# Kernel optimization log

Measured on AMD Instinct MI355X. Metric: run time of the kernel, lower is better.

Reference implementation:

```python
import jax, jax.numpy as jnp
import numpy as np

B, T, C = 2, 2048, 1024
NH = 16
HD = C // NH

def setup_inputs() -> dict:
    key = jax.random.key(0)
    ks = jax.random.split(key, 4)
    x = jax.random.normal(ks[0], (B, T, C), dtype=jnp.float32)
    w_attn = jax.random.normal(ks[1], (C, 3 * C), dtype=jnp.float32) * (1.0 / np.sqrt(C))
    b_attn = jnp.zeros((3 * C,), dtype=jnp.float32)
    w_proj = jax.random.normal(ks[2], (C, C), dtype=jnp.float32) * (1.0 / np.sqrt(C))
    b_proj = jnp.zeros((C,), dtype=jnp.float32)
    return {"x": x, "w_attn": w_attn, "b_attn": b_attn, "w_proj": w_proj, "b_proj": b_proj}

def reference(x, w_attn, b_attn, w_proj, b_proj):
    Bq, Tq, Cq = x.shape
    qkv = x @ w_attn + b_attn                      # [B,T,3C]
    q, k, v = jnp.split(qkv, 3, axis=2)
    # [B,T,C] -> [B,NH,T,HD]
    def heads(t):
        return t.reshape(Bq, Tq, NH, HD).transpose(0, 2, 1, 3)
    q, k, v = heads(q), heads(k), heads(v)
    att = jnp.einsum('bhqd,bhkd->bhqk', q, k) * (1.0 / np.sqrt(HD))
    causal = jnp.tril(jnp.ones((Tq, Tq), dtype=bool))
    att = jnp.where(causal[None, None], att, -jnp.inf)
    att = jax.nn.softmax(att, axis=-1)
    y = jnp.einsum('bhqk,bhkd->bhqd', att, v)      # [B,NH,T,HD]
    y = y.transpose(0, 2, 1, 3).reshape(Bq, Tq, Cq)
    return y @ w_proj + b_proj
```

## Files before the change

### kernel.cpp

```cpp
#include <hip/hip_runtime.h>

typedef unsigned short u16;
typedef short bf16x8 __attribute__((ext_vector_type(8)));
typedef float f32x4 __attribute__((ext_vector_type(4)));

#define BATCH 2
#define SEQ   2048
#define CH    1024
#define NHEAD 16
#define HDIM  64
#define ROWS  (BATCH*SEQ)

#define SWZ(r_, c_) (((r_)*64) + ((c_) ^ (((r_)&7)*8)))

__device__ __forceinline__ u16 f2b(float f) {
  unsigned u = __builtin_bit_cast(unsigned, f);
  u += 0x7FFFu + ((u >> 16) & 1u);
  return (u16)(u >> 16);
}
__device__ __forceinline__ float b2f(u16 h) {
  unsigned u = ((unsigned)h) << 16;
  return __builtin_bit_cast(float, u);
}
__device__ __forceinline__ float exp2_fast(float x) {
  float r; asm("v_exp_f32 %0, %1" : "=v"(r) : "v"(x)); return r;
}
__device__ __forceinline__ unsigned cvt_pk_bf16(float a, float b) {
  unsigned r; asm("v_cvt_pk_bf16_f32 %0, %1, %2" : "=v"(r) : "v"(a), "v"(b)); return r;
}

__device__ __forceinline__ void gload_lds16(const void* g, void* l) {
  __builtin_amdgcn_global_load_lds(
      (const __attribute__((address_space(1))) unsigned int*)g,
      (__attribute__((address_space(3))) unsigned int*)l, 16, 0, 0);
}

__global__ void csa_convert_x(const float* __restrict__ in, u16* __restrict__ out,
                              int n8) {
  int i = blockIdx.x * 256 + threadIdx.x;
  if (i >= n8) return;
  const float4* f4 = (const float4*)in;
  float4 v0 = f4[2*i], v1 = f4[2*i+1];
  ushort4 o0, o1;
  o0.x = f2b(v0.x); o0.y = f2b(v0.y); o0.z = f2b(v0.z); o0.w = f2b(v0.w);
  o1.x = f2b(v1.x); o1.y = f2b(v1.y); o1.z = f2b(v1.z); o1.w = f2b(v1.w);
  ((ushort4*)out)[2*i]   = o0;
  ((ushort4*)out)[2*i+1] = o1;
}

__global__ void csa_transpose2(const float* __restrict__ wa, const float* __restrict__ wp,
                               u16* __restrict__ wat, u16* __restrict__ wpt) {
  __shared__ float tile[32][33];
  int bx = blockIdx.x;
  const float* in; u16* out; int C;
  if (bx < 96) { in = wa; out = wat; C = 3*CH; }
  else         { in = wp; out = wpt; C = CH; bx -= 96; }
  const int R = CH;
  const int bxc = bx * 32, by = blockIdx.y * 32;
  const int tx = threadIdx.x, ty = threadIdx.y;
  #pragma unroll
  for (int j = 0; j < 4; ++j) {
    int r = by + ty + j*8, c = bxc + tx;
    tile[ty + j*8][tx] = in[(size_t)r*C + c];
  }
  __syncthreads();
  #pragma unroll
  for (int j = 0; j < 4; ++j) {
    int oc = bxc + ty + j*8;
    int orr = by + tx;
    out[(size_t)oc*R + orr] = f2b(tile[tx][ty + j*8]);
  }
}

__global__ __launch_bounds__(512) void csa_gemm_qkv(
    const u16* __restrict__ A, const u16* __restrict__ Bt,
    const float* __restrict__ bias,
    u16* __restrict__ qbo, u16* __restrict__ kb, u16* __restrict__ vtb)
{
  __shared__ __align__(16) u16 As[2][256*64];
  __shared__ __align__(16) u16 Bs[2][192*64];
  const int t = threadIdx.x, lane = t & 63, w = t >> 6;
  const int wm = w >> 2, wn = w & 3, g = lane >> 4, qi = lane & 15;

  const int wgid = blockIdx.y * 16 + blockIdx.x;
  const int c8 = wgid & 7, inner = wgid >> 3;
  const int bm = (c8 >> 1) * 4 + (inner >> 3);
  const int bn = (c8 & 1) * 8 + (inner & 7);

  f32x4 acc[8][3] = {};

  const u16* Ab = A  + (size_t)(bm*256)*CH;
  const u16* Bb = Bt + (size_t)(bn*192)*CH;
  const int srow = t >> 3;
  const int scol = (t & 7) * 8;

  #pragma unroll
  for (int p = 0; p < 4; ++p)
    gload_lds16(Ab + (size_t)(p*64 + srow)*CH + scol, &As[0][p*4096 + w*512]);
  #pragma unroll
  for (int p = 0; p < 3; ++p)
    gload_lds16(Bb + (size_t)(p*64 + srow)*CH + scol, &Bs[0][p*4096 + w*512]);
  __syncthreads();

  int cur = 0;
  for (int k0 = 0; k0 < CH; k0 += 64) {
    if (k0 + 64 < CH) {
      #pragma unroll
      for (int p = 0; p < 4; ++p)
        gload_lds16(Ab + (size_t)(p*64 + srow)*CH + (k0+64) + scol, &As[cur^1][p*4096 + w*512]);
      #pragma unroll
      for (int p = 0; p < 3; ++p)
        gload_lds16(Bb + (size_t)(p*64 + srow)*CH + (k0+64) + scol, &Bs[cur^1][p*4096 + w*512]);
    }
    #pragma unroll
    for (int kk = 0; kk < 2; ++kk) {
      bf16x8 af[8], bfr[3];
      #pragma unroll
      for (int m = 0; m < 8; ++m)
        af[m] = *(const bf16x8*)&As[cur][(wm*128 + m*16 + qi)*64 + kk*32 + g*8];
      #pragma unroll
      for (int n = 0; n < 3; ++n)
        bfr[n] = *(const bf16x8*)&Bs[cur][(wn*48 + n*16 + qi)*64 + kk*32 + g*8];
      #pragma unroll
      for (int m = 0; m < 8; ++m)
        #pragma unroll
        for (int n = 0; n < 3; ++n)
          acc[m][n] = __builtin_amdgcn_mfma_f32_16x16x32_bf16(af[m], bfr[n], acc[m][n], 0, 0, 0);
    }
    __syncthreads();
    cur ^= 1;
  }

  #pragma unroll
  for (int m = 0; m < 8; ++m) {
    const int row0 = bm*256 + wm*128 + m*16 + g*4;
    const int bb = row0 >> 11;
    const int t0 = row0 & 2047;
    #pragma unroll
    for (int n = 0; n < 3; ++n) {
      const int col = bn*192 + wn*48 + n*16 + qi;
      const float bv = bias[col];
      const int which = col >> 10;
      const int cc = col & 1023;
      const int h = cc >> 6, d = cc & 63;
      const int bh = bb*16 + h;
      if (which == 2) {
        ushort4 pw;
        pw.x = f2b(acc[m][n][0] + bv);
        pw.y = f2b(acc[m][n][1] + bv);
        pw.z = f2b(acc[m][n][2] + bv);
        pw.w = f2b(acc[m][n][3] + bv);
        *(ushort4*)&vtb[((size_t)bh*HDIM + d)*SEQ + t0] = pw;
      } else {
        u16* dst = (which == 0) ? qbo : kb;
        #pragma unroll
        for (int r = 0; r < 4; ++r)
          dst[((size_t)bh*SEQ + t0 + r)*HDIM + d] = f2b(acc[m][n][r] + bv);
      }
    }
  }
}

__global__ __launch_bounds__(256) void csa_gemm_proj(
    const u16* __restrict__ A, const u16* __restrict__ Bt,
    const float* __restrict__ bias, float* __restrict__ out)
{
  __shared__ __align__(16) u16 As[2][128*64];
  __shared__ __align__(16) u16 Bs[2][128*64];
  const int t = threadIdx.x, lane = t & 63, w = t >> 6;
  const int wm = w >> 1, wn = w & 1, g = lane >> 4, qi = lane & 15;
  const int bm = blockIdx.y, bn = blockIdx.x;

  f32x4 acc[4][4] = {};

  const u16* Ab = A  + (size_t)(bm*128)*CH;
  const u16* Bb = Bt + (size_t)(bn*128)*CH;
  const int srow = t >> 3;
  const int scol = (t & 7) * 8;

  #pragma unroll
  for (int p = 0; p < 4; ++p) {
    gload_lds16(Ab + (size_t)(p*32 + srow)*CH + scol, &As[0][p*2048 + w*512]);
    gload_lds16(Bb + (size_t)(p*32 + srow)*CH + scol, &Bs[0][p*2048 + w*512]);
  }
  __syncthreads();

  int cur = 0;
  for (int k0 = 0; k0 < CH; k0 += 64) {
    if (k0 + 64 < CH) {
      #pragma unroll
      for (int p = 0; p < 4; ++p) {
        gload_lds16(Ab + (size_t)(p*32 + srow)*CH + (k0+64) + scol, &As[cur^1][p*2048 + w*512]);
        gload_lds16(Bb + (size_t)(p*32 + srow)*CH + (k0+64) + scol, &Bs[cur^1][p*2048 + w*512]);
      }
    }
    #pragma unroll
    for (int kk = 0; kk < 2; ++kk) {
      bf16x8 af[4], bfr[4];
      #pragma unroll
      for (int m = 0; m < 4; ++m)
        af[m] = *(const bf16x8*)&As[cur][(wm*64 + m*16 + qi)*64 + kk*32 + g*8];
      #pragma unroll
      for (int n = 0; n < 4; ++n)
        bfr[n] = *(const bf16x8*)&Bs[cur][(wn*64 + n*16 + qi)*64 + kk*32 + g*8];
      #pragma unroll
      for (int m = 0; m < 4; ++m)
        #pragma unroll
        for (int n = 0; n < 4; ++n)
          acc[m][n] = __builtin_amdgcn_mfma_f32_16x16x32_bf16(af[m], bfr[n], acc[m][n], 0, 0, 0);
    }
    __syncthreads();
    cur ^= 1;
  }

  #pragma unroll
  for (int m = 0; m < 4; ++m) {
    const int row0 = bm*128 + wm*64 + m*16 + g*4;
    #pragma unroll
    for (int n = 0; n < 4; ++n) {
      const int col = bn*128 + wn*64 + n*16 + qi;
      const float bv = bias[col];
      #pragma unroll
      for (int r = 0; r < 4; ++r)
        out[(size_t)(row0 + r)*CH + col] = acc[m][n][r] + bv;
    }
  }
}

__global__ __launch_bounds__(512) void csa_attn(
    const u16* __restrict__ qb, const u16* __restrict__ kb,
    const u16* __restrict__ vtb, u16* __restrict__ yout)
{
  const int bh = blockIdx.x, pair = blockIdx.y;
  const int bidx = bh >> 4, h = bh & 15;
  const int t = threadIdx.x, lane = t & 63, w = t >> 6;
  const int g = lane >> 4, qi = lane & 15;
  __shared__ __align__(16) u16 Ks[2][64*64];
  __shared__ __align__(16) u16 Vs[3][64*64];
  __shared__ __align__(16) u16 Ps[8][16*64];

  const size_t kvbase = (size_t)bh * SEQ * HDIM;
  const int srow = t >> 3;
  const int ssw  = (srow & 7) * 8;
  const int scol = ((t & 7) * 8) ^ ssw;

  int offK[2][4], offPw[4], offPr[2];
  #pragma unroll
  for (int c = 0; c < 2; ++c) {
    offPr[c] = SWZ(qi, c*32 + g*8);
    #pragma unroll
    for (int s4 = 0; s4 < 4; ++s4) offK[c][s4] = SWZ(s4*16 + qi, c*32 + g*8);
  }
  #pragma unroll
  for (int s4 = 0; s4 < 4; ++s4) offPw[s4] = SWZ(qi, s4*16 + g*4);

  const float QSCALE = 0.18033688011112042f;

  for (int half = 0; half < 2; ++half) {
    const int qt = half ? (15 - pair) : pair;
    const int qrow = qt*128 + w*16;
    const int nkt = 2*qt + 2;
    const int kend = qrow >> 6;

    bf16x8 qf[2];
    #pragma unroll
    for (int c = 0; c < 2; ++c) {
      qf[c] = *(const bf16x8*)&qb[(kvbase + (size_t)(qrow + qi)*HDIM) + c*32 + g*8];
      #pragma unroll
      for (int e = 0; e < 8; ++e)
        qf[c][e] = (short)f2b(b2f((u16)qf[c][e]) * QSCALE);
    }

    f32x4 yacc[4] = {};
    float mrun = -1e30f, srun = 0.f;

    gload_lds16(kb  + kvbase + (size_t)srow*HDIM + scol, &Ks[0][w*512]);
    gload_lds16(vtb + kvbase + (size_t)srow*SEQ  + scol, &Vs[0][w*512]);
    __syncthreads();
    if (nkt > 1) {
      gload_lds16(kb  + kvbase + (size_t)(64 + srow)*HDIM + scol, &Ks[1][w*512]);
      gload_lds16(vtb + kvbase + (size_t)srow*SEQ + 64 + scol,    &Vs[1][w*512]);
    }
    f32x4 st[4] = {};
    #pragma unroll
    for (int c = 0; c < 2; ++c)
      #pragma unroll
      for (int s4 = 0; s4 < 4; ++s4) {
        bf16x8 kf = *(const bf16x8*)&Ks[0][offK[c][s4]];
        st[s4] = __builtin_amdgcn_mfma_f32_16x16x32_bf16(kf, qf[c], st[s4], 0, 0, 0);
      }

    int v0i = 0, v2i = 2;
    for (int kt = 0; kt < nkt; ++kt) {
      __syncthreads();

      if (kt + 2 < nkt) {
        const int k2 = (kt + 2) * 64;
        gload_lds16(kb  + kvbase + (size_t)(k2 + srow)*HDIM + scol, &Ks[kt & 1][w*512]);
        gload_lds16(vtb + kvbase + (size_t)srow*SEQ + k2 + scol,    &Vs[v2i][w*512]);
      }

      f32x4 st2[4] = {};
      const bool doqk = (kt + 1 <= kend);
      if (doqk) {
        #pragma unroll
        for (int c = 0; c < 2; ++c)
          #pragma unroll
          for (int s4 = 0; s4 < 4; ++s4) {
            bf16x8 kf = *(const bf16x8*)&Ks[(kt + 1) & 1][offK[c][s4]];
            st2[s4] = __builtin_amdgcn_mfma_f32_16x16x32_bf16(kf, qf[c], st2[s4], 0, 0, 0);
          }
      }

      if (kt <= kend) {
        if (kt == kend) {
          const int lq = (qrow & 63) + qi;
          #pragma unroll
          for (int s4 = 0; s4 < 4; ++s4)
            #pragma unroll
            for (int r = 0; r < 4; ++r)
              if (s4*16 + g*4 + r > lq) st[s4][r] = -3.0e38f;
        }

        float m0 = fmaxf(fmaxf(fmaxf(st[0][0], st[0][1]), st[0][2]), st[0][3]);
        float m1 = fmaxf(fmaxf(fmaxf(st[1][0], st[1][1]), st[1][2]), st[1][3]);
        float m2 = fmaxf(fmaxf(fmaxf(st[2][0], st[2][1]), st[2][2]), st[2][3]);
        float m3 = fmaxf(fmaxf(fmaxf(st[3][0], st[3][1]), st[3][2]), st[3][3]);
        float tmax = fmaxf(fmaxf(fmaxf(m0, m1), m2), m3);

        if (!__all(tmax - mrun <= 11.5f)) {
          float tmf = fmaxf(tmax, __shfl_xor(tmax, 16));
          tmf = fmaxf(tmf, __shfl_xor(tmf, 32));
          float mnew = fmaxf(mrun, tmf);
          float fac = exp2_fast(mrun - mnew);
          #pragma unroll
          for (int r = 0; r < 4; ++r) {
            float fr = __shfl(fac, g*4 + r);
            #pragma unroll
            for (int nf = 0; nf < 4; ++nf) yacc[nf][r] *= fr;
          }
          srun *= fac;
          mrun = mnew;
        }
        float tsum = 0.f;
        #pragma unroll
        for (int s4 = 0; s4 < 4; ++s4)
          #pragma unroll
          for (int r = 0; r < 4; ++r) {
            float pv = exp2_fast(st[s4][r] - mrun);
            st[s4][r] = pv;
            tsum += pv;
          }
        srun += tsum;

        #pragma unroll
        for (int s4 = 0; s4 < 4; ++s4) {
          uint2 pw;
          pw.x = cvt_pk_bf16(st[s4][0], st[s4][1]);
          pw.y = cvt_pk_bf16(st[s4][2], st[s4][3]);
          *(uint2*)&Ps[w][offPw[s4]] = pw;
        }

        __builtin_amdgcn_s_setprio(1);
        #pragma unroll
        for (int c = 0; c < 2; ++c) {
          bf16x8 pa = *(const bf16x8*)&Ps[w][offPr[c]];
          #pragma unroll
          for (int nf = 0; nf < 4; ++nf) {
            bf16x8 vf = *(const bf16x8*)&Vs[v0i][offK[c][nf]];
            yacc[nf] = __builtin_amdgcn_mfma_f32_16x16x32_bf16(pa, vf, yacc[nf], 0, 0, 0);
          }
        }
        __builtin_amdgcn_s_setprio(0);
      }

      if (doqk) {
        #pragma unroll
        for (int s4 = 0; s4 < 4; ++s4) st[s4] = st2[s4];
      }
      v0i = (v0i == 2) ? 0 : v0i + 1;
      v2i = (v2i == 2) ? 0 : v2i + 1;
    }

    float srf = srun + __shfl_xor(srun, 16);
    srf += __shfl_xor(srf, 32);
    #pragma unroll
    for (int r = 0; r < 4; ++r) {
      float sv = __shfl(srf, g*4 + r);
      float inv = 1.f / sv;
      int qg = qrow + g*4 + r;
      #pragma unroll
      for (int nf = 0; nf < 4; ++nf) {
        int d = nf*16 + qi;
        yout[((size_t)bidx*SEQ + qg)*CH + h*HDIM + d] = f2b(yacc[nf][r] * inv);
      }
    }
  }
}

extern "C" void kernel_launch(void* const* d_in, const int* in_sizes, int n_in,
                              void* d_out, int out_size, void* d_ws, size_t ws_size,
                              hipStream_t stream) {
  (void)in_sizes; (void)n_in; (void)out_size; (void)ws_size;
  const float* x      = (const float*)d_in[0];
  const float* w_attn = (const float*)d_in[1];
  const float* b_attn = (const float*)d_in[2];
  const float* w_proj = (const float*)d_in[3];
  const float* b_proj = (const float*)d_in[4];

  char* ws = (char*)d_ws;
  const size_t MB = 1024*1024;
  u16* xb  = (u16*)(ws);
  u16* wat = (u16*)(ws +  8*MB);
  u16* wpt = (u16*)(ws + 14*MB);
  u16* qb  = (u16*)(ws + 16*MB);
  u16* kb  = (u16*)(ws + 24*MB);
  u16* vtb = (u16*)(ws + 32*MB);

  csa_convert_x<<<2048, 256, 0, stream>>>(x, xb, ROWS*CH/8);
  csa_transpose2<<<dim3(128, 32), dim3(32, 8), 0, stream>>>(w_attn, w_proj, wat, wpt);
  csa_gemm_qkv<<<dim3(16, 16), 512, 0, stream>>>(xb, wat, b_attn, qb, kb, vtb);
  csa_attn<<<dim3(32, 8), 512, 0, stream>>>(qb, kb, vtb, xb);
  csa_gemm_proj<<<dim3(8, 32), 256, 0, stream>>>(xb, wpt, b_proj, (float*)d_out);
}
```

Measured before the change: 119.4 us.

## Process 128-key tiles per iteration with double-buffered K/V in attention

Restructures the causal attention loop to process 128 keys per iteration as two 64-key halves, with a simple double buffer for K and V instead of the previous 64-key tile loop with a triple-buffered V and software-pipelined QK. This halves the number of iterations and barriers, and turns the per-tile softmax max and rescale into one pass over 128 keys. In exchange it drops the QK-ahead pipelining and the early skip of fully masked 64-key tiles, so the diagonal tile may do wasted work. It also uses more LDS, which may reduce occupancy.

After: 110.9 us. -7.1%, faster.

```diff
diff --git a/kernel.cpp b/kernel.cpp
--- a/kernel.cpp
+++ b/kernel.cpp
@@ -235,32 +235,41 @@
   const int bidx = bh >> 4, h = bh & 15;
   const int t = threadIdx.x, lane = t & 63, w = t >> 6;
   const int g = lane >> 4, qi = lane & 15;
-  __shared__ __align__(16) u16 Ks[2][64*64];
-  __shared__ __align__(16) u16 Vs[3][64*64];
-  __shared__ __align__(16) u16 Ps[8][16*64];
+  __shared__ __align__(16) u16 Ks[2][128*64];
+  __shared__ __align__(16) u16 Vs[2][64*128];
+  __shared__ __align__(16) u16 Ps[8][2][16*64];
 
   const size_t kvbase = (size_t)bh * SEQ * HDIM;
-  const int srow = t >> 3;
-  const int ssw  = (srow & 7) * 8;
-  const int scol = ((t & 7) * 8) ^ ssw;
-
-  int offK[2][4], offPw[4], offPr[2];
+  const u16* kb_bh  = kb  + kvbase;
+  const u16* vtb_bh = vtb + kvbase;
+
+  const int krow_  = t >> 3;
+  const int kcolsw = ((t & 7) * 8) ^ ((krow_ & 7) * 8);
+  const int vd_    = t >> 4;
+  const int vcolsw = ((t & 15) * 8) ^ ((vd_ & 15) * 8);
+
+  int offKb[2][4], offVb[2][4], offPw[4], offPr[2];
   #pragma unroll
   for (int c = 0; c < 2; ++c) {
-    offPr[c] = SWZ(qi, c*32 + g*8);
-    #pragma unroll
-    for (int s4 = 0; s4 < 4; ++s4) offK[c][s4] = SWZ(s4*16 + qi, c*32 + g*8);
-  }
-  #pragma unroll
-  for (int s4 = 0; s4 < 4; ++s4) offPw[s4] = SWZ(qi, s4*16 + g*4);
+    offPr[c] = qi*64 + ((c*32 + g*8) ^ ((qi & 7) * 8));
+    #pragma unroll
+    for (int s4 = 0; s4 < 4; ++s4)
+      offKb[c][s4] = (s4*16 + qi)*64 + ((c*32 + g*8) ^ ((qi & 7) * 8));
+    #pragma unroll
+    for (int nf = 0; nf < 4; ++nf)
+      offVb[c][nf] = (nf*16 + qi)*128 + ((c*32 + g*8) ^ (qi * 8));
+  }
+  #pragma unroll
+  for (int s4 = 0; s4 < 4; ++s4)
+    offPw[s4] = qi*64 + ((s4*16 + g*4) ^ ((qi & 7) * 8));
 
   const float QSCALE = 0.18033688011112042f;
+  const int lqa = w*16 + qi;
 
   for (int half = 0; half < 2; ++half) {
     const int qt = half ? (15 - pair) : pair;
     const int qrow = qt*128 + w*16;
-    const int nkt = 2*qt + 2;
-    const int kend = qrow >> 6;
+    const int ntile = qt + 1;
 
     bf16x8 qf[2];
     #pragma unroll
@@ -274,112 +283,115 @@
     f32x4 yacc[4] = {};
     float mrun = -1e30f, srun = 0.f;
 
-    gload_lds16(kb  + kvbase + (size_t)srow*HDIM + scol, &Ks[0][w*512]);
-    gload_lds16(vtb + kvbase + (size_t)srow*SEQ  + scol, &Vs[0][w*512]);
     __syncthreads();
-    if (nkt > 1) {
-      gload_lds16(kb  + kvbase + (size_t)(64 + srow)*HDIM + scol, &Ks[1][w*512]);
-      gload_lds16(vtb + kvbase + (size_t)srow*SEQ + 64 + scol,    &Vs[1][w*512]);
-    }
-    f32x4 st[4] = {};
-    #pragma unroll
-    for (int c = 0; c < 2; ++c)
-      #pragma unroll
-      for (int s4 = 0; s4 < 4; ++s4) {
-        bf16x8 kf = *(const bf16x8*)&Ks[0][offK[c][s4]];
-        st[s4] = __builtin_amdgcn_mfma_f32_16x16x32_bf16(kf, qf[c], st[s4], 0, 0, 0);
-      }
-
-    int v0i = 0, v2i = 2;
-    for (int kt = 0; kt < nkt; ++kt) {
-      __syncthreads();
-
-      if (kt + 2 < nkt) {
-        const int k2 = (kt + 2) * 64;
-        gload_lds16(kb  + kvbase + (size_t)(k2 + srow)*HDIM + scol, &Ks[kt & 1][w*512]);
-        gload_lds16(vtb + kvbase + (size_t)srow*SEQ + k2 + scol,    &Vs[v2i][w*512]);
-      }
-
-      f32x4 st2[4] = {};
-      const bool doqk = (kt + 1 <= kend);
-      if (doqk) {
-        #pragma unroll
-        for (int c = 0; c < 2; ++c)
-          #pragma unroll
-          for (int s4 = 0; s4 < 4; ++s4) {
-            bf16x8 kf = *(const bf16x8*)&Ks[(kt + 1) & 1][offK[c][s4]];
-            st2[s4] = __builtin_amdgcn_mfma_f32_16x16x32_bf16(kf, qf[c], st2[s4], 0, 0, 0);
-          }
-      }
-
-      if (kt <= kend) {
-        if (kt == kend) {
-          const int lq = (qrow & 63) + qi;
-          #pragma unroll
-          for (int s4 = 0; s4 < 4; ++s4)
-            #pragma unroll
-            for (int r = 0; r < 4; ++r)
-              if (s4*16 + g*4 + r > lq) st[s4][r] = -3.0e38f;
-        }
-
-        float m0 = fmaxf(fmaxf(fmaxf(st[0][0], st[0][1]), st[0][2]), st[0][3]);
-        float m1 = fmaxf(fmaxf(fmaxf(st[1][0], st[1][1]), st[1][2]), st[1][3]);
-        float m2 = fmaxf(fmaxf(fmaxf(st[2][0], st[2][1]), st[2][2]), st[2][3]);
-        float m3 = fmaxf(fmaxf(fmaxf(st[3][0], st[3][1]), st[3][2]), st[3][3]);
-        float tmax = fmaxf(fmaxf(fmaxf(m0, m1), m2), m3);
-
-        if (!__all(tmax - mrun <= 11.5f)) {
-          float tmf = fmaxf(tmax, __shfl_xor(tmax, 16));
-          tmf = fmaxf(tmf, __shfl_xor(tmf, 32));
-          float mnew = fmaxf(mrun, tmf);
-          float fac = exp2_fast(mrun - mnew);
-          #pragma unroll
-          for (int r = 0; r < 4; ++r) {
-            float fr = __shfl(fac, g*4 + r);
-            #pragma unroll
-            for (int nf = 0; nf < 4; ++nf) yacc[nf][r] *= fr;
-          }
-          srun *= fac;
-          mrun = mnew;
-        }
-        float tsum = 0.f;
+    {
+      const u16* kp = kb_bh;
+      gload_lds16(kp + (size_t)krow_*64 + kcolsw,        &Ks[0][       w*512]);
+      gload_lds16(kp + (size_t)(64 + krow_)*64 + kcolsw, &Ks[0][4096 + w*512]);
+      const u16* vp = vtb_bh;
+      gload_lds16(vp + (size_t)vd_*SEQ + vcolsw,         &Vs[0][       w*512]);
+      gload_lds16(vp + (size_t)(32 + vd_)*SEQ + vcolsw,  &Vs[0][4096 + w*512]);
+    }
+    __syncthreads();
+
+    int buf = 0;
+    for (int kt = 0; kt < ntile; ++kt) {
+      if (kt + 1 < ntile) {
+        const u16* kp = kb_bh + (size_t)((kt + 1) * 128) * 64;
+        gload_lds16(kp + (size_t)krow_*64 + kcolsw,        &Ks[buf^1][       w*512]);
+        gload_lds16(kp + (size_t)(64 + krow_)*64 + kcolsw, &Ks[buf^1][4096 + w*512]);
+        const u16* vp = vtb_bh + (kt + 1) * 128;
+        gload_lds16(vp + (size_t)vd_*SEQ + vcolsw,         &Vs[buf^1][       w*512]);
+        gload_lds16(vp + (size_t)(32 + vd_)*SEQ + vcolsw,  &Vs[buf^1][4096 + w*512]);
+      }
+
+      f32x4 sa[4] = {}, sb[4] = {};
+      #pragma unroll
+      for (int c = 0; c < 2; ++c)
+        #pragma unroll
+        for (int s4 = 0; s4 < 4; ++s4) {
+          bf16x8 ka = *(const bf16x8*)&Ks[buf][offKb[c][s4]];
+          sa[s4] = __builtin_amdgcn_mfma_f32_16x16x32_bf16(ka, qf[c], sa[s4], 0, 0, 0);
+        }
+      #pragma unroll
+      for (int c = 0; c < 2; ++c)
+        #pragma unroll
+        for (int s4 = 0; s4 < 4; ++s4) {
+          bf16x8 kbv = *(const bf16x8*)&Ks[buf][4096 + offKb[c][s4]];
+          sb[s4] = __builtin_amdgcn_mfma_f32_16x16x32_bf16(kbv, qf[c], sb[s4], 0, 0, 0);
+        }
+
+      if (kt == ntile - 1) {
         #pragma unroll
         for (int s4 = 0; s4 < 4; ++s4)
           #pragma unroll
           for (int r = 0; r < 4; ++r) {
-            float pv = exp2_fast(st[s4][r] - mrun);
-            st[s4][r] = pv;
-            tsum += pv;
+            const int lk = s4*16 + g*4 + r;
+            if (lk > lqa)      sa[s4][r] = -3.0e38f;
+            if (lk > lqa - 64) sb[s4][r] = -3.0e38f;
           }
-        srun += tsum;
-
-        #pragma unroll
-        for (int s4 = 0; s4 < 4; ++s4) {
-          uint2 pw;
-          pw.x = cvt_pk_bf16(st[s4][0], st[s4][1]);
-          pw.y = cvt_pk_bf16(st[s4][2], st[s4][3]);
-          *(uint2*)&Ps[w][offPw[s4]] = pw;
-        }
-
-        __builtin_amdgcn_s_setprio(1);
-        #pragma unroll
-        for (int c = 0; c < 2; ++c) {
-          bf16x8 pa = *(const bf16x8*)&Ps[w][offPr[c]];
+      }
+
+      float tmax = sa[0][0];
+      #pragma unroll
+      for (int s4 = 0; s4 < 4; ++s4)
+        #pragma unroll
+        for (int r = 0; r < 4; ++r) {
+          tmax = fmaxf(tmax, sa[s4][r]);
+          tmax = fmaxf(tmax, sb[s4][r]);
+        }
+      if (!__all(tmax - mrun <= 11.5f)) {
+        float tmf = fmaxf(tmax, __shfl_xor(tmax, 16));
+        tmf = fmaxf(tmf, __shfl_xor(tmf, 32));
+        float mnew = fmaxf(mrun, tmf);
+        float fac = exp2_fast(mrun - mnew);
+        #pragma unroll
+        for (int r = 0; r < 4; ++r) {
+          float fr = __shfl(fac, g*4 + r);
           #pragma unroll
-          for (int nf = 0; nf < 4; ++nf) {
-            bf16x8 vf = *(const bf16x8*)&Vs[v0i][offK[c][nf]];
-            yacc[nf] = __builtin_amdgcn_mfma_f32_16x16x32_bf16(pa, vf, yacc[nf], 0, 0, 0);
-          }
-        }
-        __builtin_amdgcn_s_setprio(0);
-      }
-
-      if (doqk) {
-        #pragma unroll
-        for (int s4 = 0; s4 < 4; ++s4) st[s4] = st2[s4];
-      }
-      v0i = (v0i == 2) ? 0 : v0i + 1;
-      v2i = (v2i == 2) ? 0 : v2i + 1;
+          for (int nf = 0; nf < 4; ++nf) yacc[nf][r] *= fr;
+        }
+        srun *= fac;
+        mrun = mnew;
+      }
+      float tsum = 0.f;
+      #pragma unroll
+      for (int s4 = 0; s4 < 4; ++s4)
+        #pragma unroll
+        for (int r = 0; r < 4; ++r) {
+          float pa = exp2_fast(sa[s4][r] - mrun);
+          float pb = exp2_fast(sb[s4][r] - mrun);
+          sa[s4][r] = pa; sb[s4][r] = pb;
+          tsum += pa + pb;
+        }
+      srun += tsum;
+
+      #pragma unroll
+      for (int s4 = 0; s4 < 4; ++s4) {
+        uint2 pwa, pwb;
+        pwa.x = cvt_pk_bf16(sa[s4][0], sa[s4][1]);
+        pwa.y = cvt_pk_bf16(sa[s4][2], sa[s4][3]);
+        pwb.x = cvt_pk_bf16(sb[s4][0], sb[s4][1]);
+        pwb.y = cvt_pk_bf16(sb[s4][2], sb[s4][3]);
+        *(uint2*)&Ps[w][0][offPw[s4]] = pwa;
+        *(uint2*)&Ps[w][1][offPw[s4]] = pwb;
+      }
+
+      #pragma unroll
+      for (int c = 0; c < 2; ++c) {
+        bf16x8 pa0 = *(const bf16x8*)&Ps[w][0][offPr[c]];
+        bf16x8 pb0 = *(const bf16x8*)&Ps[w][1][offPr[c]];
+        #pragma unroll
+        for (int nf = 0; nf < 4; ++nf) {
+          bf16x8 va = *(const bf16x8*)&Vs[buf][offVb[c][nf]];
+          yacc[nf] = __builtin_amdgcn_mfma_f32_16x16x32_bf16(pa0, va, yacc[nf], 0, 0, 0);
+          bf16x8 vb = *(const bf16x8*)&Vs[buf][offVb[c][nf] ^ 64];
+          yacc[nf] = __builtin_amdgcn_mfma_f32_16x16x32_bf16(pb0, vb, yacc[nf], 0, 0, 0);
+        }
+      }
+
+      __syncthreads();
+      buf ^= 1;
     }
 
     float srf = srun + __shfl_xor(srun, 16);
```
